# Optimization experiments

Hardware: AMD Instinct MI355X
Metric: run time of the kernel (lower is better)

## Reference

```python
import jax, jax.numpy as jnp
import numpy as np

C, T, B, F = 3, 100, 512, 128
HX, HZ, H, EH, L = 128, 128, 256, 128, 64


def setup_inputs() -> dict:
    key = jax.random.key(0)
    ks = jax.random.split(key, 20)
    n = lambda k, s: jax.random.normal(k, s, jnp.float32) * 0.05
    return {
        "x": jax.random.normal(ks[0], (C, T, B, F), jnp.float32),
        "phi_x_W": n(ks[1], (C, F, HX)),
        "phi_x_b": n(ks[2], (C, HX)),
        "enc_W": n(ks[3], (C, HX + H, EH)),
        "enc_b": n(ks[4], (C, EH)),
        "enc_mu_W": n(ks[5], (C, EH, L)),
        "enc_mu_b": n(ks[6], (C, L)),
        "phi_z_W": n(ks[7], (L, HZ)),
        "phi_z_b": n(ks[8], (HZ,)),
        "dec_W": n(ks[9], (C, HZ + H, EH)),
        "dec_b": n(ks[10], (C, EH)),
        "dec_mu_W": n(ks[11], (C, EH, F)),
        "dec_mu_b": n(ks[12], (C, F)),
        "rnn_Wih": n(ks[13], (HX + HZ, H)),
        "rnn_Whh": n(ks[14], (H, H)),
        "rnn_bih": n(ks[15], (H,)),
        "rnn_bhh": n(ks[16], (H,)),
        "h0": jnp.zeros((C, B, H), jnp.float32),
    }


def reference(x, phi_x_W, phi_x_b, enc_W, enc_b, enc_mu_W, enc_mu_b,
              phi_z_W, phi_z_b, dec_W, dec_b, dec_mu_W, dec_mu_b,
              rnn_Wih, rnn_Whh, rnn_bih, rnn_bhh, h0):
    # Eval-mode forward of MCRNNVAE ('long' channels): per channel, per timestep:
    # phi_x (Linear) -> encoder([phi_x, h]) -> z = mu (deterministic eval)
    # -> phi_z (Linear) -> decoder([phi_z, h]) -> RNN h update on [phi_x, phi_z].
    # NOTE: PhiBlock/VariationalBlock hidden layers have NO nonlinearity in source.
    outs = []
    for c in range(x.shape[0]):  # small fixed channel loop
        Wx, bx = phi_x_W[c], phi_x_b[c]
        We, be = enc_W[c], enc_b[c]
        Wqm, bqm = enc_mu_W[c], enc_mu_b[c]
        Wd, bd = dec_W[c], dec_b[c]
        Wpm, bpm = dec_mu_W[c], dec_mu_b[c]

        def step(h, xt):
            x_phi = xt @ Wx + bx                                    # [B,HX]
            e = jnp.concatenate([x_phi, h], axis=-1) @ We + be      # [B,EH]
            z = e @ Wqm + bqm                                       # z = qzx.loc, [B,L]
            z_phi = z @ phi_z_W + phi_z_b                           # [B,HZ]
            d = jnp.concatenate([z_phi, h], axis=-1) @ Wd + bd      # [B,EH]
            mu_p = d @ Wpm + bpm                                    # recon mean [B,F]
            rnn_in = jnp.concatenate([x_phi, z_phi], axis=-1)       # [B,HX+HZ]
            h_new = jnp.tanh(rnn_in @ rnn_Wih + rnn_bih + h @ rnn_Whh + rnn_bhh)
            return h_new, mu_p

        _, mus = jax.lax.scan(step, h0[c], x[c])  # mus: [T,B,F]
        outs.append(mus)
    return jnp.stack(outs)  # [C,T,B,F]
```

## Files before the change

kernel.cpp:

```cpp
#include <hip/hip_runtime.h>
#include <hip/hip_bf16.h>
#include <cstdint>


typedef __attribute__((ext_vector_type(8))) short short8;
typedef __attribute__((ext_vector_type(4))) float float4v;

__device__ __forceinline__ float bf2f(unsigned short u){
  union { unsigned int i; float f; } v; v.i = ((unsigned int)u) << 16; return v.f;
}
__device__ __forceinline__ unsigned short f2bf(float f){
  union { float f; unsigned int i; } v; v.f = f;
  unsigned int r = v.i + 0x7fffu + ((v.i >> 16) & 1u);
  return (unsigned short)(r >> 16);
}
__device__ __forceinline__ void st_bf2(unsigned short* p, float a, float b){
  unsigned int pa = f2bf(a), pb = f2bf(b);
  *(unsigned int*)p = pa | (pb << 16);
}
__device__ __forceinline__ float ftanh(float x){
  x = fminf(15.f, fmaxf(-15.f, x));
  float e = __expf(2.f * x);
  return (e - 1.f) * __builtin_amdgcn_rcpf(e + 1.f);
}

__device__ __forceinline__ float dotSB(const float* __restrict__ a,
                                       const float* __restrict__ b, int K, int ldb){
  float s = 0.f;
  #pragma unroll 4
  for (int k = 0; k < K; ++k) s = fmaf(a[k], b[(size_t)k * ldb], s);
  return s;
}

__global__ void pre1(const float* __restrict__ encW, const float* __restrict__ encb,
                     const float* __restrict__ Wqm, const float* __restrict__ bqm,
                     float* __restrict__ T1, float* __restrict__ T2, float* __restrict__ c0a){
  int i = blockIdx.x * 256 + threadIdx.x;
  if (i < 24576){
    int c = i >> 13, rr = (i >> 6) & 127, l = i & 63;
    T1[i] = dotSB(encW + ((size_t)c*384 + rr)*128, Wqm + (size_t)c*8192 + l, 128, 64);
  } else if (i < 73728){
    int j = i - 24576; int c = j >> 14, rr = (j >> 6) & 255, l = j & 63;
    T2[j] = dotSB(encW + ((size_t)c*384 + 128 + rr)*128, Wqm + (size_t)c*8192 + l, 128, 64);
  } else if (i < 73920){
    int j = i - 73728; int c = j >> 6, l = j & 63;
    c0a[j] = dotSB(encb + c*128, Wqm + (size_t)c*8192 + l, 128, 64) + bqm[j];
  }
}

__global__ void pre2(const float* __restrict__ T1, const float* __restrict__ T2,
                     const float* __restrict__ c0a, const float* __restrict__ Wz,
                     const float* __restrict__ bz,
                     float* __restrict__ A, float* __restrict__ Bm, float* __restrict__ c0){
  int i = blockIdx.x * 256 + threadIdx.x;
  if (i < 49152){
    int c = i >> 14, rr = (i >> 7) & 127, n = i & 127;
    A[i] = dotSB(T1 + ((size_t)c*128 + rr)*64, Wz + n, 64, 128);
  } else if (i < 147456){
    int j = i - 49152; int c = j >> 15, rr = (j >> 7) & 255, n = j & 127;
    Bm[j] = dotSB(T2 + ((size_t)c*256 + rr)*64, Wz + n, 64, 128);
  } else if (i < 147840){
    int j = i - 147456; int c = j >> 7, n = j & 127;
    c0[j] = dotSB(c0a + c*64, Wz + n, 64, 128) + bz[n];
  }
}

__global__ void pre3(const float* __restrict__ A, const float* __restrict__ Bm,
                     const float* __restrict__ c0, const float* __restrict__ Wih,
                     const float* __restrict__ Whh, const float* __restrict__ bih,
                     const float* __restrict__ bhh, const float* __restrict__ decW,
                     const float* __restrict__ decb,
                     float* __restrict__ P, float* __restrict__ Q, float* __restrict__ r,
                     float* __restrict__ D1, float* __restrict__ E1, float* __restrict__ m0a){
  int i = blockIdx.x * 256 + threadIdx.x;
  const float* Wi2 = Wih + 128*256;
  if (i < 98304){
    int c = i >> 15, rr = (i >> 8) & 127, n = i & 255;
    P[i] = Wih[rr*256 + n] + dotSB(A + ((size_t)c*128 + rr)*128, Wi2 + n, 128, 256);
  } else if (i < 294912){
    int j = i - 98304; int c = j >> 16, rr = (j >> 8) & 255, n = j & 255;
    Q[j] = Whh[rr*256 + n] + dotSB(Bm + ((size_t)c*256 + rr)*128, Wi2 + n, 128, 256);
  } else if (i < 295680){
    int j = i - 294912; int c = j >> 8, n = j & 255;
    r[j] = dotSB(c0 + c*128, Wi2 + n, 128, 256) + bih[n] + bhh[n];
  } else if (i < 344832){
    int j = i - 295680; int c = j >> 14, rr = (j >> 7) & 127, n = j & 127;
    D1[j] = dotSB(A + ((size_t)c*128 + rr)*128, decW + (size_t)c*49152 + n, 128, 128);
  } else if (i < 443136){
    int j = i - 344832; int c = j >> 15, rr = (j >> 7) & 255, n = j & 127;
    E1[j] = decW[(size_t)c*49152 + (size_t)(128 + rr)*128 + n]
          + dotSB(Bm + ((size_t)c*256 + rr)*128, decW + (size_t)c*49152 + n, 128, 128);
  } else if (i < 443520){
    int j = i - 443136; int c = j >> 7, n = j & 127;
    m0a[j] = dotSB(c0 + c*128, decW + (size_t)c*49152 + n, 128, 128) + decb[j];
  }
}

__global__ void pre4(const float* __restrict__ Wx, const float* __restrict__ bx,
                     const float* __restrict__ P, const float* __restrict__ r,
                     const float* __restrict__ D1, const float* __restrict__ E1,
                     const float* __restrict__ m0a, const float* __restrict__ Wpm,
                     const float* __restrict__ bpm,
                     float* __restrict__ R, float* __restrict__ r0,
                     float* __restrict__ M1, float* __restrict__ M2, float* __restrict__ m0){
  int i = blockIdx.x * 256 + threadIdx.x;
  if (i < 98304){
    int c = i >> 15, rr = (i >> 8) & 127, n = i & 255;
    R[i] = dotSB(Wx + ((size_t)c*128 + rr)*128, P + (size_t)c*32768 + n, 128, 256);
  } else if (i < 99072){
    int j = i - 98304; int c = j >> 8, n = j & 255;
    r0[j] = dotSB(bx + c*128, P + (size_t)c*32768 + n, 128, 256) + r[j];
  } else if (i < 148224){
    int j = i - 99072; int c = j >> 14, rr = (j >> 7) & 127, n = j & 127;
    M1[j] = dotSB(D1 + ((size_t)c*128 + rr)*128, Wpm + (size_t)c*16384 + n, 128, 128);
  } else if (i < 246528){
    int j = i - 148224; int c = j >> 15, rr = (j >> 7) & 255, n = j & 127;
    M2[j] = dotSB(E1 + ((size_t)c*256 + rr)*128, Wpm + (size_t)c*16384 + n, 128, 128);
  } else if (i < 246912){
    int j = i - 246528; int c = j >> 7, n = j & 127;
    m0[j] = dotSB(m0a + c*128, Wpm + (size_t)c*16384 + n, 128, 128) + bpm[j];
  }
}

__global__ void pre5(const float* __restrict__ Wx, const float* __restrict__ bx,
                     const float* __restrict__ M1, const float* __restrict__ m0,
                     float* __restrict__ Nn, float* __restrict__ n0){
  int i = blockIdx.x * 256 + threadIdx.x;
  if (i < 49152){
    int c = i >> 14, rr = (i >> 7) & 127, n = i & 127;
    Nn[i] = dotSB(Wx + ((size_t)c*128 + rr)*128, M1 + (size_t)c*16384 + n, 128, 128);
  } else if (i < 49536){
    int j = i - 49152; int c = j >> 7, n = j & 127;
    n0[j] = dotSB(bx + c*128, M1 + (size_t)c*16384 + n, 128, 128) + m0[j];
  }
}

#define MFMA_BF16 __builtin_amdgcn_mfma_f32_16x16x32_bf16

__global__ __launch_bounds__(512, 2)
void kernU2(const float* __restrict__ x, const float* __restrict__ Rg,
            const float* __restrict__ r0g, unsigned short* __restrict__ U){
  __shared__ unsigned short xs[128][136];
  const int m0 = blockIdx.x * 128;
  const int c  = m0 / 51200;
  const int w  = threadIdx.x >> 6;
  const int l  = threadIdx.x & 63;
  const int q  = l >> 4, m = l & 15;
  const float* __restrict__ Rc = Rg + (size_t)c * 32768;

  short8 rf[4][2];
  #pragma unroll
  for (int kt = 0; kt < 4; ++kt)
    #pragma unroll
    for (int nt = 0; nt < 2; ++nt){
      union { short8 v; unsigned short u[8]; } tmp;
      const int col = 32*w + 16*nt + m;
      #pragma unroll
      for (int j = 0; j < 8; ++j)
        tmp.u[j] = f2bf(Rc[(size_t)(32*kt + 8*q + j)*256 + col]);
      rf[kt][nt] = tmp.v;
    }
  const float r0v0 = r0g[c*256 + 32*w + m];
  const float r0v1 = r0g[c*256 + 32*w + 16 + m];

  {
    const int r  = threadIdx.x >> 2;
    const int c0 = (threadIdx.x & 3) * 32;
    const float* xr = x + (size_t)(m0 + r)*128 + c0;
    #pragma unroll
    for (int i = 0; i < 8; ++i){
      float4 v = *(const float4*)(xr + 4*i);
      st_bf2(&xs[r][c0 + 4*i],     v.x, v.y);
      st_bf2(&xs[r][c0 + 4*i + 2], v.z, v.w);
    }
  }
  __syncthreads();

  #pragma unroll 1
  for (int mt = 0; mt < 8; ++mt){
    float4v a0 = { r0v0, r0v0, r0v0, r0v0 };
    float4v a1 = { r0v1, r0v1, r0v1, r0v1 };
    #pragma unroll
    for (int kt = 0; kt < 4; ++kt){
      short8 af = *(const short8*)&xs[16*mt + m][32*kt + 8*q];
      a0 = MFMA_BF16(af, rf[kt][0], a0, 0,0,0);
      a1 = MFMA_BF16(af, rf[kt][1], a1, 0,0,0);
    }
    unsigned short* ub = U + (size_t)(m0 + 16*mt + 4*q)*256;
    ub[0*256 + 32*w + m]      = f2bf(a0.x);
    ub[1*256 + 32*w + m]      = f2bf(a0.y);
    ub[2*256 + 32*w + m]      = f2bf(a0.z);
    ub[3*256 + 32*w + m]      = f2bf(a0.w);
    ub[0*256 + 32*w + 16 + m] = f2bf(a1.x);
    ub[1*256 + 32*w + 16 + m] = f2bf(a1.y);
    ub[2*256 + 32*w + 16 + m] = f2bf(a1.z);
    ub[3*256 + 32*w + 16 + m] = f2bf(a1.w);
  }
}

__global__ __launch_bounds__(512, 2)
void kernB2(const unsigned short* __restrict__ U, const float* __restrict__ Qg,
            const float* __restrict__ h0, unsigned short* __restrict__ Hs){
  __shared__ unsigned short hHi[16][264];
  __shared__ unsigned short hLo[16][264];
  const int c  = blockIdx.x >> 5;
  const int b0 = (blockIdx.x & 31) << 4;
  const int w  = threadIdx.x >> 6;
  const int l  = threadIdx.x & 63;
  const int q  = l >> 4, m = l & 15;
  const float* __restrict__ Qc = Qg + (size_t)c * 65536;

  short8 qf[8][2];
  #pragma unroll
  for (int kt = 0; kt < 8; ++kt)
    #pragma unroll
    for (int nt = 0; nt < 2; ++nt){
      union { short8 v; unsigned short u[8]; } tmp;
      const int col = 32*w + 16*nt + m;
      #pragma unroll
      for (int j = 0; j < 8; ++j)
        tmp.u[j] = f2bf(Qc[(size_t)(32*kt + 8*q + j)*256 + col]);
      qf[kt][nt] = tmp.v;
    }

  unsigned short hiR[8];
  #pragma unroll
  for (int nt = 0; nt < 2; ++nt){
    const int col = 32*w + 16*nt + m;
    #pragma unroll
    for (int r = 0; r < 4; ++r){
      const int row = 4*q + r;
      float v = h0[((size_t)c*512 + b0 + row)*256 + col];
      unsigned short hi = f2bf(v);
      hiR[nt*4 + r] = hi;
      hHi[row][col] = hi;
      hLo[row][col] = f2bf(v - bf2f(hi));
    }
  }
  __syncthreads();

  unsigned short un[8];
  #pragma unroll
  for (int nt = 0; nt < 2; ++nt)
    #pragma unroll
    for (int r = 0; r < 4; ++r)
      un[nt*4 + r] = U[((size_t)(c*100 + 0)*512 + b0 + 4*q + r)*256 + 32*w + 16*nt + m];

  #pragma unroll 1
  for (int t = 0; t < 100; ++t){
    const size_t rowbase = (size_t)(c*100 + t)*512 + b0;
    #pragma unroll
    for (int nt = 0; nt < 2; ++nt)
      #pragma unroll
      for (int r = 0; r < 4; ++r)
        Hs[(rowbase + 4*q + r)*256 + 32*w + 16*nt + m] = hiR[nt*4 + r];

    float4v acc0 = { bf2f(un[0]), bf2f(un[1]), bf2f(un[2]), bf2f(un[3]) };
    float4v acc1 = { bf2f(un[4]), bf2f(un[5]), bf2f(un[6]), bf2f(un[7]) };

    const int tn = (t < 99) ? t + 1 : 99;
    #pragma unroll
    for (int nt = 0; nt < 2; ++nt)
      #pragma unroll
      for (int r = 0; r < 4; ++r)
        un[nt*4 + r] = U[((size_t)(c*100 + tn)*512 + b0 + 4*q + r)*256 + 32*w + 16*nt + m];

    #pragma unroll
    for (int kt = 0; kt < 8; ++kt){
      short8 ahi = *(const short8*)&hHi[m][32*kt + 8*q];
      short8 alo = *(const short8*)&hLo[m][32*kt + 8*q];
      acc0 = MFMA_BF16(ahi, qf[kt][0], acc0, 0,0,0);
      acc1 = MFMA_BF16(ahi, qf[kt][1], acc1, 0,0,0);
      acc0 = MFMA_BF16(alo, qf[kt][0], acc0, 0,0,0);
      acc1 = MFMA_BF16(alo, qf[kt][1], acc1, 0,0,0);
    }

    float hn[8];
    hn[0] = ftanh(acc0.x); hn[1] = ftanh(acc0.y); hn[2] = ftanh(acc0.z); hn[3] = ftanh(acc0.w);
    hn[4] = ftanh(acc1.x); hn[5] = ftanh(acc1.y); hn[6] = ftanh(acc1.z); hn[7] = ftanh(acc1.w);

    __syncthreads();
    #pragma unroll
    for (int nt = 0; nt < 2; ++nt){
      const int col = 32*w + 16*nt + m;
      #pragma unroll
      for (int r = 0; r < 4; ++r){
        const int row = 4*q + r;
        float v = hn[nt*4 + r];
        unsigned short hi = f2bf(v);
        hiR[nt*4 + r] = hi;
        hHi[row][col] = hi;
        hLo[row][col] = f2bf(v - bf2f(hi));
      }
    }
    __syncthreads();
  }
}

__global__ __launch_bounds__(512, 2)
void kernC3(const float* __restrict__ x, const unsigned short* __restrict__ Hs,
            const float* __restrict__ Nn, const float* __restrict__ M2,
            const float* __restrict__ n0, float* __restrict__ out){
  __shared__ unsigned short xs[128][136];
  const int m0 = blockIdx.x * 128;
  const int c  = m0 / 51200;
  const int w  = threadIdx.x >> 6;
  const int l  = threadIdx.x & 63;
  const int q  = l >> 4, m = l & 15;
  const int col = 16*w + m;
  const float* __restrict__ Nc  = Nn + (size_t)c * 16384;
  const float* __restrict__ M2c = M2 + (size_t)c * 32768;

  short8 bw[12];
  #pragma unroll
  for (int kt = 0; kt < 4; ++kt){
    union { short8 v; unsigned short u[8]; } tmp;
    #pragma unroll
    for (int j = 0; j < 8; ++j)
      tmp.u[j] = f2bf(Nc[(size_t)(32*kt + 8*q + j)*128 + col]);
    bw[kt] = tmp.v;
  }
  #pragma unroll
  for (int kt = 0; kt < 8; ++kt){
    union { short8 v; unsigned short u[8]; } tmp;
    #pragma unroll
    for (int j = 0; j < 8; ++j)
      tmp.u[j] = f2bf(M2c[(size_t)(32*kt + 8*q + j)*128 + col]);
    bw[4 + kt] = tmp.v;
  }
  const float nz = n0[c*128 + col];

  {
    const int r  = threadIdx.x >> 2;
    const int c0 = (threadIdx.x & 3) * 32;
    const float* xr = x + (size_t)(m0 + r)*128 + c0;
    #pragma unroll
    for (int i = 0; i < 8; ++i){
      float4 v = *(const float4*)(xr + 4*i);
      st_bf2(&xs[r][c0 + 4*i],     v.x, v.y);
      st_bf2(&xs[r][c0 + 4*i + 2], v.z, v.w);
    }
  }
  __syncthreads();

  #pragma unroll 1
  for (int mt = 0; mt < 8; ++mt){
    float4v aa = { nz, nz, nz, nz }, ab = { 0.f, 0.f, 0.f, 0.f };
    #pragma unroll
    for (int kt = 0; kt < 4; ++kt){
      short8 af = *(const short8*)&xs[16*mt + m][32*kt + 8*q];
      if (kt & 1) ab = MFMA_BF16(af, bw[kt], ab, 0,0,0);
      else        aa = MFMA_BF16(af, bw[kt], aa, 0,0,0);
    }
    const size_t mrow = (size_t)(m0 + 16*mt) + m;
    #pragma unroll
    for (int kt = 0; kt < 8; ++kt){
      short8 af = *(const short8*)&Hs[mrow*256 + 32*kt + 8*q];
      if (kt & 1) ab = MFMA_BF16(af, bw[4+kt], ab, 0,0,0);
      else        aa = MFMA_BF16(af, bw[4+kt], aa, 0,0,0);
    }
    float* ob = out + (size_t)(m0 + 16*mt + 4*q)*128 + col;
    ob[0]   = aa.x + ab.x;
    ob[128] = aa.y + ab.y;
    ob[256] = aa.z + ab.z;
    ob[384] = aa.w + ab.w;
  }
}

extern "C" void kernel_launch(void* const* d_in, const int* in_sizes, int n_in,
                              void* d_out, int out_size, void* d_ws, size_t ws_size,
                              hipStream_t stream){
  const float* x    = (const float*)d_in[0];
  const float* Wx   = (const float*)d_in[1];
  const float* bx   = (const float*)d_in[2];
  const float* encW = (const float*)d_in[3];
  const float* encb = (const float*)d_in[4];
  const float* Wqm  = (const float*)d_in[5];
  const float* bqm  = (const float*)d_in[6];
  const float* Wz   = (const float*)d_in[7];
  const float* bz   = (const float*)d_in[8];
  const float* decW = (const float*)d_in[9];
  const float* decb = (const float*)d_in[10];
  const float* Wpm  = (const float*)d_in[11];
  const float* bpm  = (const float*)d_in[12];
  const float* Wih  = (const float*)d_in[13];
  const float* Whh  = (const float*)d_in[14];
  const float* bih  = (const float*)d_in[15];
  const float* bhh  = (const float*)d_in[16];
  const float* h0   = (const float*)d_in[17];

  float* ws = (float*)d_ws;
  size_t off = 0;
  auto alloc = [&](size_t n){ float* p = ws + off; off += n; return p; };
  float* T1  = alloc(24576);  float* T2  = alloc(49152);  float* c0a = alloc(192);
  float* A   = alloc(49152);  float* Bm  = alloc(98304);  float* c0  = alloc(384);
  float* P   = alloc(98304);  float* Q   = alloc(196608); float* r   = alloc(768);
  float* D1  = alloc(49152);  float* E1  = alloc(98304);  float* m0a = alloc(384);
  float* R   = alloc(98304);  float* r0  = alloc(768);
  float* M1  = alloc(49152);  float* M2  = alloc(98304);  float* m0  = alloc(384);
  float* Nn  = alloc(49152);  float* n0  = alloc(384);
  unsigned short* Hs = (unsigned short*)(ws + off); off += 19660800;
  unsigned short* U  = (unsigned short*)d_out;

  hipLaunchKernelGGL(pre1, dim3(289),  dim3(256), 0, stream, encW, encb, Wqm, bqm, T1, T2, c0a);
  hipLaunchKernelGGL(pre2, dim3(578),  dim3(256), 0, stream, T1, T2, c0a, Wz, bz, A, Bm, c0);
  hipLaunchKernelGGL(pre3, dim3(1733), dim3(256), 0, stream, A, Bm, c0, Wih, Whh, bih, bhh,
                     decW, decb, P, Q, r, D1, E1, m0a);
  hipLaunchKernelGGL(pre4, dim3(965),  dim3(256), 0, stream, Wx, bx, P, r, D1, E1, m0a,
                     Wpm, bpm, R, r0, M1, M2, m0);
  hipLaunchKernelGGL(pre5, dim3(194),  dim3(256), 0, stream, Wx, bx, M1, m0, Nn, n0);
  hipLaunchKernelGGL(kernU2, dim3(1200), dim3(512), 0, stream, x, R, r0, U);
  hipLaunchKernelGGL(kernB2, dim3(96),   dim3(512), 0, stream, U, Q, h0, Hs);
  hipLaunchKernelGGL(kernC3, dim3(1200), dim3(512), 0, stream, x, Hs, Nn, M2, n0, (float*)d_out);
}
```

Baseline: 483.8 us.

## Fuse input projection into recurrent kernel with double-buffered hidden state

Removes the separate kernU2 pass that precomputed the x-projection into a bf16 buffer. The recurrent kernel now computes the projection each step from a prefetched x slice. The block grows to 1024 threads (16 waves, one 16-column tile each) and hidden state and x are double-buffered in LDS, so each step needs one barrier instead of two. This trades the U write and read traffic and a kernel launch for extra MFMA work on the serial critical path, and with only 96 blocks the recurrence stays latency-bound.

```diff
diff --git a/kernel.cpp b/kernel.cpp
--- a/kernel.cpp
+++ b/kernel.cpp
@@ -137,162 +137,109 @@
 
 #define MFMA_BF16 __builtin_amdgcn_mfma_f32_16x16x32_bf16
 
-__global__ __launch_bounds__(512, 2)
-void kernU2(const float* __restrict__ x, const float* __restrict__ Rg,
-            const float* __restrict__ r0g, unsigned short* __restrict__ U){
-  __shared__ unsigned short xs[128][136];
-  const int m0 = blockIdx.x * 128;
-  const int c  = m0 / 51200;
-  const int w  = threadIdx.x >> 6;
-  const int l  = threadIdx.x & 63;
-  const int q  = l >> 4, m = l & 15;
-  const float* __restrict__ Rc = Rg + (size_t)c * 32768;
-
-  short8 rf[4][2];
-  #pragma unroll
-  for (int kt = 0; kt < 4; ++kt)
-    #pragma unroll
-    for (int nt = 0; nt < 2; ++nt){
-      union { short8 v; unsigned short u[8]; } tmp;
-      const int col = 32*w + 16*nt + m;
-      #pragma unroll
-      for (int j = 0; j < 8; ++j)
-        tmp.u[j] = f2bf(Rc[(size_t)(32*kt + 8*q + j)*256 + col]);
-      rf[kt][nt] = tmp.v;
-    }
-  const float r0v0 = r0g[c*256 + 32*w + m];
-  const float r0v1 = r0g[c*256 + 32*w + 16 + m];
-
-  {
-    const int r  = threadIdx.x >> 2;
-    const int c0 = (threadIdx.x & 3) * 32;
-    const float* xr = x + (size_t)(m0 + r)*128 + c0;
-    #pragma unroll
-    for (int i = 0; i < 8; ++i){
-      float4 v = *(const float4*)(xr + 4*i);
-      st_bf2(&xs[r][c0 + 4*i],     v.x, v.y);
-      st_bf2(&xs[r][c0 + 4*i + 2], v.z, v.w);
-    }
-  }
-  __syncthreads();
-
-  #pragma unroll 1
-  for (int mt = 0; mt < 8; ++mt){
-    float4v a0 = { r0v0, r0v0, r0v0, r0v0 };
-    float4v a1 = { r0v1, r0v1, r0v1, r0v1 };
-    #pragma unroll
-    for (int kt = 0; kt < 4; ++kt){
-      short8 af = *(const short8*)&xs[16*mt + m][32*kt + 8*q];
-      a0 = MFMA_BF16(af, rf[kt][0], a0, 0,0,0);
-      a1 = MFMA_BF16(af, rf[kt][1], a1, 0,0,0);
-    }
-    unsigned short* ub = U + (size_t)(m0 + 16*mt + 4*q)*256;
-    ub[0*256 + 32*w + m]      = f2bf(a0.x);
-    ub[1*256 + 32*w + m]      = f2bf(a0.y);
-    ub[2*256 + 32*w + m]      = f2bf(a0.z);
-    ub[3*256 + 32*w + m]      = f2bf(a0.w);
-    ub[0*256 + 32*w + 16 + m] = f2bf(a1.x);
-    ub[1*256 + 32*w + 16 + m] = f2bf(a1.y);
-    ub[2*256 + 32*w + 16 + m] = f2bf(a1.z);
-    ub[3*256 + 32*w + 16 + m] = f2bf(a1.w);
-  }
-}
-
-__global__ __launch_bounds__(512, 2)
-void kernB2(const unsigned short* __restrict__ U, const float* __restrict__ Qg,
+__global__ __launch_bounds__(1024, 4)
+void kernBU(const float* __restrict__ x, const float* __restrict__ Rg,
+            const float* __restrict__ r0g, const float* __restrict__ Qg,
             const float* __restrict__ h0, unsigned short* __restrict__ Hs){
-  __shared__ unsigned short hHi[16][264];
-  __shared__ unsigned short hLo[16][264];
+  __shared__ unsigned short hHi[2][16][264];
+  __shared__ unsigned short hLo[2][16][264];
+  __shared__ unsigned short xsS[2][16][136];
   const int c  = blockIdx.x >> 5;
   const int b0 = (blockIdx.x & 31) << 4;
   const int w  = threadIdx.x >> 6;
   const int l  = threadIdx.x & 63;
   const int q  = l >> 4, m = l & 15;
+  const int col = 16*w + m;
   const float* __restrict__ Qc = Qg + (size_t)c * 65536;
-
-  short8 qf[8][2];
-  #pragma unroll
-  for (int kt = 0; kt < 8; ++kt)
-    #pragma unroll
-    for (int nt = 0; nt < 2; ++nt){
-      union { short8 v; unsigned short u[8]; } tmp;
-      const int col = 32*w + 16*nt + m;
-      #pragma unroll
-      for (int j = 0; j < 8; ++j)
-        tmp.u[j] = f2bf(Qc[(size_t)(32*kt + 8*q + j)*256 + col]);
-      qf[kt][nt] = tmp.v;
-    }
-
-  unsigned short hiR[8];
-  #pragma unroll
-  for (int nt = 0; nt < 2; ++nt){
-    const int col = 32*w + 16*nt + m;
+  const float* __restrict__ Rc = Rg + (size_t)c * 32768;
+
+  short8 qf[8];
+  #pragma unroll
+  for (int kt = 0; kt < 8; ++kt){
+    union { short8 v; unsigned short u[8]; } tmp;
+    #pragma unroll
+    for (int j = 0; j < 8; ++j)
+      tmp.u[j] = f2bf(Qc[(size_t)(32*kt + 8*q + j)*256 + col]);
+    qf[kt] = tmp.v;
+  }
+  short8 rf[4];
+  #pragma unroll
+  for (int kt = 0; kt < 4; ++kt){
+    union { short8 v; unsigned short u[8]; } tmp;
+    #pragma unroll
+    for (int j = 0; j < 8; ++j)
+      tmp.u[j] = f2bf(Rc[(size_t)(32*kt + 8*q + j)*256 + col]);
+    rf[kt] = tmp.v;
+  }
+  const float r0v = r0g[c*256 + col];
+
+  unsigned short hiR[4];
+  #pragma unroll
+  for (int r = 0; r < 4; ++r){
+    const int row = 4*q + r;
+    float v = h0[((size_t)c*512 + b0 + row)*256 + col];
+    unsigned short hi = f2bf(v);
+    hiR[r] = hi;
+    hHi[0][row][col] = hi;
+    hLo[0][row][col] = f2bf(v - bf2f(hi));
+  }
+  {
+    const int c0 = l * 2;
+    float2 v = *(const float2*)(x + ((size_t)(c*100 + 0)*512 + b0 + w)*128 + c0);
+    st_bf2(&xsS[0][w][c0], v.x, v.y);
+  }
+  __syncthreads();
+
+  #pragma unroll 1
+  for (int t = 0; t < 100; ++t){
+    const int cur = t & 1, nxt = cur ^ 1;
+
+    const size_t rowbase = (size_t)(c*100 + t)*512 + b0;
+    #pragma unroll
+    for (int r = 0; r < 4; ++r)
+      Hs[(rowbase + 4*q + r)*256 + col] = hiR[r];
+
+    const int tn = (t < 99) ? t + 1 : 99;
+    const int c0 = l * 2;
+    float2 xv = *(const float2*)(x + ((size_t)(c*100 + tn)*512 + b0 + w)*128 + c0);
+
+    float4v accx = { r0v, r0v, r0v, r0v };
+    float4v acch = { 0.f, 0.f, 0.f, 0.f };
+    float4v accl = { 0.f, 0.f, 0.f, 0.f };
+    #pragma unroll
+    for (int kt = 0; kt < 4; ++kt){
+      short8 ax  = *(const short8*)&xsS[cur][m][32*kt + 8*q];
+      short8 ahi = *(const short8*)&hHi[cur][m][32*kt + 8*q];
+      short8 alo = *(const short8*)&hLo[cur][m][32*kt + 8*q];
+      accx = MFMA_BF16(ax,  rf[kt], accx, 0,0,0);
+      acch = MFMA_BF16(ahi, qf[kt], acch, 0,0,0);
+      accl = MFMA_BF16(alo, qf[kt], accl, 0,0,0);
+    }
+    #pragma unroll
+    for (int kt = 4; kt < 8; ++kt){
+      short8 ahi = *(const short8*)&hHi[cur][m][32*kt + 8*q];
+      short8 alo = *(const short8*)&hLo[cur][m][32*kt + 8*q];
+      acch = MFMA_BF16(ahi, qf[kt], acch, 0,0,0);
+      accl = MFMA_BF16(alo, qf[kt], accl, 0,0,0);
+    }
+
+    float hn[4];
+    hn[0] = ftanh(accx.x + acch.x + accl.x);
+    hn[1] = ftanh(accx.y + acch.y + accl.y);
+    hn[2] = ftanh(accx.z + acch.z + accl.z);
+    hn[3] = ftanh(accx.w + acch.w + accl.w);
+
     #pragma unroll
     for (int r = 0; r < 4; ++r){
       const int row = 4*q + r;
-      float v = h0[((size_t)c*512 + b0 + row)*256 + col];
+      float v = hn[r];
       unsigned short hi = f2bf(v);
-      hiR[nt*4 + r] = hi;
-      hHi[row][col] = hi;
-      hLo[row][col] = f2bf(v - bf2f(hi));
-    }
-  }
-  __syncthreads();
-
-  unsigned short un[8];
-  #pragma unroll
-  for (int nt = 0; nt < 2; ++nt)
-    #pragma unroll
-    for (int r = 0; r < 4; ++r)
-      un[nt*4 + r] = U[((size_t)(c*100 + 0)*512 + b0 + 4*q + r)*256 + 32*w + 16*nt + m];
-
-  #pragma unroll 1
-  for (int t = 0; t < 100; ++t){
-    const size_t rowbase = (size_t)(c*100 + t)*512 + b0;
-    #pragma unroll
-    for (int nt = 0; nt < 2; ++nt)
-      #pragma unroll
-      for (int r = 0; r < 4; ++r)
-        Hs[(rowbase + 4*q + r)*256 + 32*w + 16*nt + m] = hiR[nt*4 + r];
-
-    float4v acc0 = { bf2f(un[0]), bf2f(un[1]), bf2f(un[2]), bf2f(un[3]) };
-    float4v acc1 = { bf2f(un[4]), bf2f(un[5]), bf2f(un[6]), bf2f(un[7]) };
-
-    const int tn = (t < 99) ? t + 1 : 99;
-    #pragma unroll
-    for (int nt = 0; nt < 2; ++nt)
-      #pragma unroll
-      for (int r = 0; r < 4; ++r)
-        un[nt*4 + r] = U[((size_t)(c*100 + tn)*512 + b0 + 4*q + r)*256 + 32*w + 16*nt + m];
-
-    #pragma unroll
-    for (int kt = 0; kt < 8; ++kt){
-      short8 ahi = *(const short8*)&hHi[m][32*kt + 8*q];
-      short8 alo = *(const short8*)&hLo[m][32*kt + 8*q];
-      acc0 = MFMA_BF16(ahi, qf[kt][0], acc0, 0,0,0);
-      acc1 = MFMA_BF16(ahi, qf[kt][1], acc1, 0,0,0);
-      acc0 = MFMA_BF16(alo, qf[kt][0], acc0, 0,0,0);
-      acc1 = MFMA_BF16(alo, qf[kt][1], acc1, 0,0,0);
-    }
-
-    float hn[8];
-    hn[0] = ftanh(acc0.x); hn[1] = ftanh(acc0.y); hn[2] = ftanh(acc0.z); hn[3] = ftanh(acc0.w);
-    hn[4] = ftanh(acc1.x); hn[5] = ftanh(acc1.y); hn[6] = ftanh(acc1.z); hn[7] = ftanh(acc1.w);
-
-    __syncthreads();
-    #pragma unroll
-    for (int nt = 0; nt < 2; ++nt){
-      const int col = 32*w + 16*nt + m;
-      #pragma unroll
-      for (int r = 0; r < 4; ++r){
-        const int row = 4*q + r;
-        float v = hn[nt*4 + r];
-        unsigned short hi = f2bf(v);
-        hiR[nt*4 + r] = hi;
-        hHi[row][col] = hi;
-        hLo[row][col] = f2bf(v - bf2f(hi));
-      }
-    }
+      hiR[r] = hi;
+      hHi[nxt][row][col] = hi;
+      hLo[nxt][row][col] = f2bf(v - bf2f(hi));
+    }
+    st_bf2(&xsS[nxt][w][c0], xv.x, xv.y);
+
     __syncthreads();
   }
 }
@@ -400,7 +347,6 @@
   float* M1  = alloc(49152);  float* M2  = alloc(98304);  float* m0  = alloc(384);
   float* Nn  = alloc(49152);  float* n0  = alloc(384);
   unsigned short* Hs = (unsigned short*)(ws + off); off += 19660800;
-  unsigned short* U  = (unsigned short*)d_out;
 
   hipLaunchKernelGGL(pre1, dim3(289),  dim3(256), 0, stream, encW, encb, Wqm, bqm, T1, T2, c0a);
   hipLaunchKernelGGL(pre2, dim3(578),  dim3(256), 0, stream, T1, T2, c0a, Wz, bz, A, Bm, c0);
@@ -409,7 +355,6 @@
   hipLaunchKernelGGL(pre4, dim3(965),  dim3(256), 0, stream, Wx, bx, P, r, D1, E1, m0a,
                      Wpm, bpm, R, r0, M1, M2, m0);
   hipLaunchKernelGGL(pre5, dim3(194),  dim3(256), 0, stream, Wx, bx, M1, m0, Nn, n0);
-  hipLaunchKernelGGL(kernU2, dim3(1200), dim3(512), 0, stream, x, R, r0, U);
-  hipLaunchKernelGGL(kernB2, dim3(96),   dim3(512), 0, stream, U, Q, h0, Hs);
+  hipLaunchKernelGGL(kernBU, dim3(96),   dim3(1024), 0, stream, x, R, r0, Q, h0, Hs);
   hipLaunchKernelGGL(kernC3, dim3(1200), dim3(512), 0, stream, x, Hs, Nn, M2, n0, (float*)d_out);
 }
```

Result: no change. 492.4 us (+1.8%).
